# Optimization experiments

Measured on AMD Instinct MI355X. Metric: run time of the kernel, lower is better.

Reference implementation:

```python
import jax, jax.numpy as jnp
import numpy as np

B, T, DM, D, W, DG = 2, 4096, 2048, 4096, 4, 512  # batch, seq, model hidden, conv channels (value_dim), kernel size, generator hidden


def setup_inputs() -> dict:
    key = jax.random.key(0)
    k0, k1, k2, k3, k4 = jax.random.split(key, 5)
    return {
        "x": jax.random.normal(k0, (B, T, D), jnp.float32) * 0.02,
        "generator_input": jax.random.normal(k1, (B, T, DM), jnp.float32) * 0.02,
        "w1": jax.random.normal(k2, (DG, DM), jnp.float32) * 0.02,   # Linear(DM -> DG), no bias
        "w2": jax.random.normal(k3, (D * W, DG), jnp.float32) * 0.02,  # Linear(DG -> D*W)
        "b2": jax.random.normal(k4, (D * W,), jnp.float32) * 0.02,
    }


def reference(x, generator_input, w1, w2, b2):
    # Hypernetwork: per-token depthwise conv kernels [B, T, D, W]
    h = jax.nn.silu(jnp.einsum("btm,gm->btg", generator_input, w1))
    kflat = jnp.einsum("btg,kg->btk", h, w2) + b2
    kernels = kflat.reshape(x.shape[0], x.shape[1], x.shape[2], W)
    # Causal depthwise conv: left-pad by W-1, windowed multiply-accumulate.
    xp = jnp.pad(x, ((0, 0), (W - 1, 0), (0, 0)))
    Tlen = x.shape[1]
    y = kernels[..., 0] * xp[:, 0:Tlen, :]
    for w in range(1, W):
        y = y + kernels[..., w] * xp[:, w:w + Tlen, :]
    return jax.nn.silu(y)  # [B, T, D]
```

## Files before the change

### kernel.cpp

```cpp
#include <hip/hip_runtime.h>
#include <hip/hip_bf16.h>
#include <stdint.h>

#define TLEN 4096
#define DMm  2048
#define DD   4096
#define DGg  512
#define BT   8192
#define DW   16384

typedef __attribute__((ext_vector_type(8))) short bf16x8;
typedef __attribute__((ext_vector_type(4))) float f32x4;

__device__ __forceinline__ unsigned short f2bf(float f) {
    union { float f; unsigned u; } c; c.f = f;
    unsigned u = c.u;
    unsigned r = (u + 0x7FFFu + ((u >> 16) & 1u)) >> 16;
    return (unsigned short)r;
}

__global__ void cast4_kernel(const float* __restrict__ in,
                             unsigned short* __restrict__ out, int n4) {
    int i = blockIdx.x * blockDim.x + threadIdx.x;
    if (i >= n4) return;
    float4 v = reinterpret_cast<const float4*>(in)[i];
    ushort4 o;
    o.x = f2bf(v.x); o.y = f2bf(v.y); o.z = f2bf(v.z); o.w = f2bf(v.w);
    reinterpret_cast<ushort4*>(out)[i] = o;
}

#define GLDS16(gp, lp)                                                         \
    __builtin_amdgcn_global_load_lds(                                          \
        (__attribute__((address_space(1))) const void*)(gp),                   \
        (__attribute__((address_space(3))) void*)(lp), 16, 0, 0)

#define VMCNT(n) asm volatile("s_waitcnt vmcnt(" #n ")" ::: "memory")
#define SBAR()   __builtin_amdgcn_s_barrier()
#define SCHED0() __builtin_amdgcn_sched_barrier(0)

__global__ __launch_bounds__(256) void gemm1_silu_kernel(
    const unsigned short* __restrict__ A,
    const unsigned short* __restrict__ Bm,
    unsigned short* __restrict__ H)
{
    __shared__ short smA[128 * 32];
    __shared__ short smB[128 * 32];
    const int m0   = blockIdx.y * 128;
    const int n0   = blockIdx.x * 128;
    const int lane = threadIdx.x & 63;
    const int wave = threadIdx.x >> 6;
    const int wm   = wave >> 1, wn = wave & 1;

    const int c0 = wave * 64 + lane;
    const int c1 = c0 + 256;
    const int rA0 = m0 + (c0 >> 2), rA1 = m0 + (c1 >> 2);
    const int rB0 = n0 + (c0 >> 2), rB1 = n0 + (c1 >> 2);
    const int ko0 = (c0 & 3) * 8,  ko1 = (c1 & 3) * 8;

    f32x4 acc[4][4] = {};

    for (int k0 = 0; k0 < DMm; k0 += 32) {
        GLDS16(A  + (size_t)rA0 * DMm + k0 + ko0, smA + wave * 512);
        GLDS16(A  + (size_t)rA1 * DMm + k0 + ko1, smA + 2048 + wave * 512);
        GLDS16(Bm + (size_t)rB0 * DMm + k0 + ko0, smB + wave * 512);
        GLDS16(Bm + (size_t)rB1 * DMm + k0 + ko1, smB + 2048 + wave * 512);
        __syncthreads();

        const int la = lane & 15, ko = (lane >> 4) * 8;
        bf16x8 af[4], bfr[4];
#pragma unroll
        for (int mm = 0; mm < 4; ++mm)
            af[mm] = *reinterpret_cast<const bf16x8*>(&smA[(wm * 64 + mm * 16 + la) * 32 + ko]);
#pragma unroll
        for (int nn = 0; nn < 4; ++nn)
            bfr[nn] = *reinterpret_cast<const bf16x8*>(&smB[(wn * 64 + nn * 16 + la) * 32 + ko]);
#pragma unroll
        for (int mm = 0; mm < 4; ++mm)
#pragma unroll
            for (int nn = 0; nn < 4; ++nn)
                acc[mm][nn] = __builtin_amdgcn_mfma_f32_16x16x32_bf16(
                    af[mm], bfr[nn], acc[mm][nn], 0, 0, 0);
        __syncthreads();
    }

#pragma unroll
    for (int mm = 0; mm < 4; ++mm) {
        int rowB = m0 + wm * 64 + mm * 16 + (lane >> 4) * 4;
#pragma unroll
        for (int nn = 0; nn < 4; ++nn) {
            int colG = n0 + wn * 64 + nn * 16 + (lane & 15);
#pragma unroll
            for (int j = 0; j < 4; ++j) {
                float v = acc[mm][nn][j];
                float s = v / (1.0f + __expf(-v));
                H[(size_t)(rowB + j) * DGg + colG] = f2bf(s);
            }
        }
    }
}

#define LDS_B2 65536
#define LDS_Y2 70448

__global__ __launch_bounds__(512, 2) void gemm2_conv_silu_kernel(
    const unsigned short* __restrict__ Hb,
    const unsigned short* __restrict__ W2b,
    const float* __restrict__ b2,
    const float* __restrict__ x,
    float* __restrict__ out)
{
    __shared__ __attribute__((aligned(16))) char lds[140080];
    const int tid  = threadIdx.x;
    const int lane = tid & 63, wave = tid >> 6;
    const int wm   = wave >> 2, wn = wave & 3;
    const int la   = lane & 15, hi = lane >> 4;

    int bid = blockIdx.x;
    int swz = (bid & 7) * 256 + (bid >> 3);
    const int n0 = (swz >> 5) * 256;
    const int t0 = (swz & 31) * 256;
    const int d0 = n0 >> 2;

    const int srow = lane >> 2;
    const int scol = ((lane & 3) ^ ((srow >> 1) & 3)) * 8;

    auto stageA = [&](int tk, int p) {
#pragma unroll
        for (int q = 0; q < 2; ++q) {
            int chunk = wave * 2 + q;
            int row   = chunk * 16 + srow;
            GLDS16(W2b + (size_t)(n0 + row) * DGg + tk * 32 + scol,
                   lds + p * 16384 + chunk * 1024);
        }
    };
    auto stageB = [&](int tk, int p) {
#pragma unroll
        for (int q = 0; q < 2; ++q) {
            int chunk = wave * 2 + q;
            int row   = chunk * 16 + srow;
            GLDS16(Hb + (size_t)(t0 + row) * DGg + tk * 32 + scol,
                   lds + LDS_B2 + p * 16384 + chunk * 1024);
        }
    };

    f32x4 acc[8][4] = {};
    const int slotb = (hi ^ ((la >> 1) & 3)) * 16;

    auto region = [&](int t, bool doStage) {
        const int p = t & 3;
        const char* aB = lds + p * 16384 + (wm * 128 + la) * 64 + slotb;
        const char* bB = lds + LDS_B2 + p * 16384 + (wn * 64 + la) * 64 + slotb;
        bf16x8 aF[8], bF[4];
#pragma unroll
        for (int m = 0; m < 8; ++m)
            aF[m] = *reinterpret_cast<const bf16x8*>(aB + m * 1024);
#pragma unroll
        for (int nr = 0; nr < 4; ++nr)
            bF[nr] = *reinterpret_cast<const bf16x8*>(bB + nr * 1024);
        if (doStage) { stageA(t + 3, (t + 3) & 3); stageB(t + 3, (t + 3) & 3); }
        SCHED0();
        __builtin_amdgcn_s_setprio(1);
#pragma unroll
        for (int m = 0; m < 8; ++m)
#pragma unroll
            for (int nr = 0; nr < 4; ++nr)
                acc[m][nr] = __builtin_amdgcn_mfma_f32_16x16x32_bf16(
                    aF[m], bF[nr], acc[m][nr], 0, 0, 0);
        __builtin_amdgcn_s_setprio(0);
        SCHED0();
    };

    float4 xv[9];
#pragma unroll
    for (int k = 0; k < 9; ++k) {
        int c = tid + k * 512;
        float4 v = make_float4(0.f, 0.f, 0.f, 0.f);
        if (c < 4144) {
            int row = c >> 4, q = c & 15;
            int rg = t0 - 3 + row;
            if (rg >= 0 && (rg >> 12) == (t0 >> 12))
                v = *reinterpret_cast<const float4*>(&x[(size_t)rg * DD + d0 + q * 4]);
        }
        xv[k] = v;
    }
    stageA(0, 0); stageB(0, 0);
    stageA(1, 1); stageB(1, 1);
    stageA(2, 2); stageB(2, 2);
    SCHED0();
    VMCNT(8);
    SBAR();

    for (int t = 0; t < 13; ++t) {
        region(t, true);
        VMCNT(8);
        SBAR();
    }
    region(13, false); VMCNT(4); SBAR();
    region(14, false); VMCNT(0); SBAR();
    region(15, false);

    __syncthreads();

    float* smX = reinterpret_cast<float*>(lds);
#pragma unroll
    for (int k = 0; k < 9; ++k) {
        int c = tid + k * 512;
        if (c < 4144) {
            int row = c >> 4, q = c & 15;
            *reinterpret_cast<float4*>(&smX[row * 68 + q * 4]) = xv[k];
        }
    }
    __syncthreads();

    float4 bb[8];
#pragma unroll
    for (int m = 0; m < 8; ++m)
        bb[m] = *reinterpret_cast<const float4*>(&b2[n0 + wm * 128 + m * 16 + hi * 4]);

    float* smY = reinterpret_cast<float*>(lds + LDS_Y2);
#pragma unroll
    for (int nr = 0; nr < 4; ++nr) {
        int tl = wn * 64 + nr * 16 + la;
#pragma unroll
        for (int m = 0; m < 8; ++m) {
            int dl = wm * 32 + m * 4 + hi;
            float pv =
                  (acc[m][nr][0] + bb[m].x) * smX[(tl + 0) * 68 + dl]
                + (acc[m][nr][1] + bb[m].y) * smX[(tl + 1) * 68 + dl]
                + (acc[m][nr][2] + bb[m].z) * smX[(tl + 2) * 68 + dl]
                + (acc[m][nr][3] + bb[m].w) * smX[(tl + 3) * 68 + dl];
            smY[tl * 68 + dl] = pv / (1.0f + __expf(-pv));
        }
    }
    __syncthreads();

    for (int c = tid; c < 256 * 16; c += 512) {
        int row = c >> 4, q = c & 15;
        float4 v = *reinterpret_cast<const float4*>(&smY[row * 68 + q * 4]);
        *reinterpret_cast<float4*>(&out[(size_t)(t0 + row) * DD + d0 + q * 4]) = v;
    }
}

extern "C" void kernel_launch(void* const* d_in, const int* in_sizes, int n_in,
                              void* d_out, int out_size, void* d_ws, size_t ws_size,
                              hipStream_t stream) {
    const float* x   = (const float*)d_in[0];
    const float* gen = (const float*)d_in[1];
    const float* w1  = (const float*)d_in[2];
    const float* w2  = (const float*)d_in[3];
    const float* b2  = (const float*)d_in[4];
    float* out = (float*)d_out;

    char* ws = (char*)d_ws;
    size_t off = 0;
    unsigned short* gen_b = (unsigned short*)(ws + off); off += (size_t)BT * DMm * 2;
    unsigned short* w1_b  = (unsigned short*)(ws + off); off += (size_t)DGg * DMm * 2;
    unsigned short* w2_b  = (unsigned short*)(ws + off); off += (size_t)DW * DGg * 2;
    unsigned short* h_b   = (unsigned short*)(ws + off); off += (size_t)BT * DGg * 2;

    int n4;
    n4 = BT * DMm / 4;
    cast4_kernel<<<(n4 + 255) / 256, 256, 0, stream>>>(gen, gen_b, n4);
    n4 = DGg * DMm / 4;
    cast4_kernel<<<(n4 + 255) / 256, 256, 0, stream>>>(w1, w1_b, n4);
    n4 = DW * DGg / 4;
    cast4_kernel<<<(n4 + 255) / 256, 256, 0, stream>>>(w2, w2_b, n4);

    gemm1_silu_kernel<<<dim3(DGg / 128, BT / 128), 256, 0, stream>>>(gen_b, w1_b, h_b);
    gemm2_conv_silu_kernel<<<2048, 512, 0, stream>>>(h_b, w2_b, b2, x, out);
}
```

Baseline: 285.8 us.

## Double-buffer A fragments in gemm2 and merge the three cast launches

Restructures the gemm2 main loop so the LDS reads of the A fragments for the next k-step are issued before the current step's MFMAs, using two register sets. The loads overlap with compute, and the vmcnt wait is tightened accordingly. The x-tile prefetch moves after the GEMM loop, and the three fp32-to-bf16 cast launches are fused into one kernel writing the contiguous workspace. The changes add register pressure at 2 blocks/CU and expose x-load latency after the loop.

```diff
diff --git a/kernel.cpp b/kernel.cpp
--- a/kernel.cpp
+++ b/kernel.cpp
@@ -19,14 +19,23 @@
     return (unsigned short)r;
 }
 
-__global__ void cast4_kernel(const float* __restrict__ in,
-                             unsigned short* __restrict__ out, int n4) {
+#define NB1 (BT * DMm / 4)
+#define NB2 (DGg * DMm / 4)
+#define NB3 (DW * DGg / 4)
+__global__ void cast_all_kernel(const float* __restrict__ g,
+                                const float* __restrict__ w1,
+                                const float* __restrict__ w2,
+                                unsigned short* __restrict__ o) {
     int i = blockIdx.x * blockDim.x + threadIdx.x;
-    if (i >= n4) return;
-    float4 v = reinterpret_cast<const float4*>(in)[i];
-    ushort4 o;
-    o.x = f2bf(v.x); o.y = f2bf(v.y); o.z = f2bf(v.z); o.w = f2bf(v.w);
-    reinterpret_cast<ushort4*>(out)[i] = o;
+    if (i >= NB1 + NB2 + NB3) return;
+    const float* src; int j = i;
+    if (j < NB1) { src = g; }
+    else if (j < NB1 + NB2) { src = w1; j -= NB1; }
+    else { src = w2; j -= NB1 + NB2; }
+    float4 v = reinterpret_cast<const float4*>(src)[j];
+    ushort4 u;
+    u.x = f2bf(v.x); u.y = f2bf(v.y); u.z = f2bf(v.z); u.w = f2bf(v.w);
+    reinterpret_cast<ushort4*>(o)[i] = u;
 }
 
 #define GLDS16(gp, lp)                                                         \
@@ -100,7 +109,6 @@
 }
 
 #define LDS_B2 65536
-#define LDS_Y2 70448
 
 __global__ __launch_bounds__(512, 2) void gemm2_conv_silu_kernel(
     const unsigned short* __restrict__ Hb,
@@ -127,8 +135,7 @@
     auto stageA = [&](int tk, int p) {
 #pragma unroll
         for (int q = 0; q < 2; ++q) {
-            int chunk = wave * 2 + q;
-            int row   = chunk * 16 + srow;
+            int chunk = wave * 2 + q, row = chunk * 16 + srow;
             GLDS16(W2b + (size_t)(n0 + row) * DGg + tk * 32 + scol,
                    lds + p * 16384 + chunk * 1024);
         }
@@ -136,8 +143,7 @@
     auto stageB = [&](int tk, int p) {
 #pragma unroll
         for (int q = 0; q < 2; ++q) {
-            int chunk = wave * 2 + q;
-            int row   = chunk * 16 + srow;
+            int chunk = wave * 2 + q, row = chunk * 16 + srow;
             GLDS16(Hb + (size_t)(t0 + row) * DGg + tk * 32 + scol,
                    lds + LDS_B2 + p * 16384 + chunk * 1024);
         }
@@ -145,19 +151,27 @@
 
     f32x4 acc[8][4] = {};
     const int slotb = (hi ^ ((la >> 1) & 3)) * 16;
-
-    auto region = [&](int t, bool doStage) {
-        const int p = t & 3;
-        const char* aB = lds + p * 16384 + (wm * 128 + la) * 64 + slotb;
-        const char* bB = lds + LDS_B2 + p * 16384 + (wn * 64 + la) * 64 + slotb;
-        bf16x8 aF[8], bF[4];
+    const int aOff  = (wm * 128 + la) * 64 + slotb;
+    const int bOff  = (wn * 64 + la) * 64 + slotb;
+
+    bf16x8 aFa[8], aFb[8];
+
+    auto rdA = [&](bf16x8 (&dst)[8], int p) {
+        const char* aB = lds + p * 16384 + aOff;
 #pragma unroll
         for (int m = 0; m < 8; ++m)
-            aF[m] = *reinterpret_cast<const bf16x8*>(aB + m * 1024);
+            dst[m] = *reinterpret_cast<const bf16x8*>(aB + m * 1024);
+    };
+
+    auto body = [&](bf16x8 (&AC)[8], bf16x8 (&AN)[8], int pcur, int pnext,
+                    int tkS, bool doStage, bool doPre) {
+        bf16x8 bF[4];
+        const char* bB = lds + LDS_B2 + pcur * 16384 + bOff;
 #pragma unroll
         for (int nr = 0; nr < 4; ++nr)
             bF[nr] = *reinterpret_cast<const bf16x8*>(bB + nr * 1024);
-        if (doStage) { stageA(t + 3, (t + 3) & 3); stageB(t + 3, (t + 3) & 3); }
+        if (doPre) rdA(AN, pnext);
+        if (doStage) { stageA(tkS, tkS & 3); stageB(tkS, tkS & 3); }
         SCHED0();
         __builtin_amdgcn_s_setprio(1);
 #pragma unroll
@@ -165,10 +179,28 @@
 #pragma unroll
             for (int nr = 0; nr < 4; ++nr)
                 acc[m][nr] = __builtin_amdgcn_mfma_f32_16x16x32_bf16(
-                    aF[m], bF[nr], acc[m][nr], 0, 0, 0);
+                    AC[m], bF[nr], acc[m][nr], 0, 0, 0);
         __builtin_amdgcn_s_setprio(0);
         SCHED0();
     };
+
+    stageA(0, 0); stageB(0, 0);
+    stageA(1, 1); stageB(1, 1);
+    stageA(2, 2); stageB(2, 2);
+    VMCNT(4);
+    SBAR();
+    rdA(aFa, 0);
+
+#pragma unroll
+    for (int r = 0; r < 13; ++r) {
+        if (r & 1) body(aFb, aFa, r & 3, (r + 1) & 3, r + 3, true, true);
+        else       body(aFa, aFb, r & 3, (r + 1) & 3, r + 3, true, true);
+        VMCNT(4);
+        SBAR();
+    }
+    body(aFb, aFa, 1, 2, 0, false, true);  VMCNT(0); SBAR();
+    body(aFa, aFb, 2, 3, 0, false, true);  SBAR();
+    body(aFb, aFa, 3, 0, 0, false, false);
 
     float4 xv[9];
 #pragma unroll
@@ -183,22 +215,6 @@
         }
         xv[k] = v;
     }
-    stageA(0, 0); stageB(0, 0);
-    stageA(1, 1); stageB(1, 1);
-    stageA(2, 2); stageB(2, 2);
-    SCHED0();
-    VMCNT(8);
-    SBAR();
-
-    for (int t = 0; t < 13; ++t) {
-        region(t, true);
-        VMCNT(8);
-        SBAR();
-    }
-    region(13, false); VMCNT(4); SBAR();
-    region(14, false); VMCNT(0); SBAR();
-    region(15, false);
-
     __syncthreads();
 
     float* smX = reinterpret_cast<float*>(lds);
@@ -217,7 +233,7 @@
     for (int m = 0; m < 8; ++m)
         bb[m] = *reinterpret_cast<const float4*>(&b2[n0 + wm * 128 + m * 16 + hi * 4]);
 
-    float* smY = reinterpret_cast<float*>(lds + LDS_Y2);
+    float* smY = reinterpret_cast<float*>(lds + 70448);
 #pragma unroll
     for (int nr = 0; nr < 4; ++nr) {
         int tl = wn * 64 + nr * 16 + la;
@@ -258,13 +274,8 @@
     unsigned short* w2_b  = (unsigned short*)(ws + off); off += (size_t)DW * DGg * 2;
     unsigned short* h_b   = (unsigned short*)(ws + off); off += (size_t)BT * DGg * 2;
 
-    int n4;
-    n4 = BT * DMm / 4;
-    cast4_kernel<<<(n4 + 255) / 256, 256, 0, stream>>>(gen, gen_b, n4);
-    n4 = DGg * DMm / 4;
-    cast4_kernel<<<(n4 + 255) / 256, 256, 0, stream>>>(w1, w1_b, n4);
-    n4 = DW * DGg / 4;
-    cast4_kernel<<<(n4 + 255) / 256, 256, 0, stream>>>(w2, w2_b, n4);
+    int total4 = NB1 + NB2 + NB3;
+    cast_all_kernel<<<(total4 + 255) / 256, 256, 0, stream>>>(gen, w1, w2, gen_b);
 
     gemm1_silu_kernel<<<dim3(DGg / 128, BT / 128), 256, 0, stream>>>(gen_b, w1_b, h_b);
     gemm2_conv_silu_kernel<<<2048, 512, 0, stream>>>(h_b, w2_b, b2, x, out);
```

Measured after the change: 261.1 us. -8.7%, faster.
